# Kernel optimization log

Measured on AMD Instinct MI355X. Metric: run time of the kernel, lower is better.

Reference implementation:

```python
import jax, jax.numpy as jnp
import numpy as np

WS = 8          # window_size
HEADS = 6
DH = 32         # dim_head


def _dwconv(t, w):
    # t: (B,C,H,W), w: (C,1,3,3) depthwise, stride 1, padding 1 -> SAME
    return jax.lax.conv_general_dilated(
        t, w, window_strides=(1, 1), padding='SAME',
        feature_group_count=t.shape[1],
        dimension_numbers=('NCHW', 'OIHW', 'NCHW'))


def _l2norm(t, eps=1e-12):
    # matches F.normalize: x / max(||x||, eps)
    n = jnp.sqrt(jnp.sum(t * t, axis=-1, keepdims=True))
    return t / jnp.maximum(n, eps)


def setup_inputs() -> dict:
    key = jax.random.key(0)
    ks = jax.random.split(key, 10)
    B, H, W, C = 2, 256, 256, 192
    s = 0.05
    return {
        'x': jax.random.normal(ks[0], (B, H, W, C), jnp.float32),
        'illu_fea_trans': jax.random.normal(ks[1], (B, H, W, C), jnp.float32),
        'gt_w': jax.random.normal(ks[2], (C, C), jnp.float32) * s,
        'gt_b': jax.random.normal(ks[3], (C,), jnp.float32) * s,
        'qkv_w': jax.random.normal(ks[4], (C, 3 * C), jnp.float32) * s,
        'qkv_b': jax.random.normal(ks[5], (3 * C,), jnp.float32) * s,
        'proj_w': jax.random.normal(ks[6], (C, C), jnp.float32) * s,
        'proj_b': jax.random.normal(ks[7], (C,), jnp.float32) * s,
        'conv1_w': jax.random.normal(ks[8], (C, 1, 3, 3), jnp.float32) * s,
        'conv2_w': jax.random.normal(ks[9], (C, 1, 3, 3), jnp.float32) * s,
    }


def reference(x, illu_fea_trans, gt_w, gt_b, qkv_w, qkv_b, proj_w, proj_b,
              conv1_w, conv2_w):
    B, H, W, C = x.shape
    Ws, heads, d = WS, HEADS, DH
    scale = d ** (-0.5)
    pad_h = (Ws - H % Ws) % Ws
    pad_w = (Ws - W % Ws) % Ws
    xp = jnp.pad(x, ((0, 0), (0, pad_h), (0, pad_w), (0, 0)), mode='reflect')
    ip = jnp.pad(illu_fea_trans, ((0, 0), (0, pad_h), (0, pad_w), (0, 0)), mode='reflect')
    Hp, Wp = xp.shape[1], xp.shape[2]
    nW = (Hp // Ws) * (Wp // Ws)
    T = Ws * Ws

    def to_windows(t):
        t = t.reshape(B, Hp // Ws, Ws, Wp // Ws, Ws, C)
        return t.transpose(0, 1, 3, 2, 4, 5).reshape(B * nW, T, C)

    xw = to_windows(xp)                                  # (B*nW, T, C)
    qkv = (xw @ qkv_w + qkv_b).reshape(B * nW, T, 3, heads, d)
    qkv = qkv.transpose(2, 0, 3, 1, 4)                   # (3, Bn, h, T, d)
    q, k, v = qkv[0], qkv[1], qkv[2]
    q = _l2norm(q)
    k = _l2norm(k)

    illu = to_windows(ip).reshape(B * nW, T, heads, d).transpose(0, 2, 1, 3)
    v = v * (1.0 + jax.nn.sigmoid(illu))

    # global token: avg-pool over padded spatial dims, then linear
    gt = jnp.mean(xp, axis=(1, 2)) @ gt_w + gt_b          # (B, C)
    gt = gt.reshape(B, heads, 1, d)
    # faithful to torch expand(dim=2 -> nW).reshape(B*nW, heads, 1, d)
    gk = jnp.broadcast_to(gt, (B, heads, nW, d)).reshape(B * nW, heads, 1, d)
    k = jnp.concatenate([k, gk], axis=2)                  # (Bn, h, T+1, d)
    v = jnp.concatenate([v, gk], axis=2)

    # chunked softmax over keys == full softmax over key axis (chunks on q only)
    attn = jax.nn.softmax(jnp.einsum('bhqd,bhkd->bhqk', q, k) * scale, axis=-1)
    out = jnp.einsum('bhqk,bhkd->bhqd', attn, v)          # (Bn, h, T, d)
    out = out.transpose(0, 2, 1, 3).reshape(B * nW, T, C)
    out = out @ proj_w + proj_b

    out = out.reshape(B, Hp // Ws, Wp // Ws, Ws, Ws, C)
    out = out.transpose(0, 1, 3, 2, 4, 5).reshape(B, Hp, Wp, C)[:, :H, :W, :]

    # depthwise-conv positional branch on padded x (exact gelu like torch)
    t = xp.transpose(0, 3, 1, 2)                          # (B,C,Hp,Wp)
    t = _dwconv(t, conv1_w)
    t = jax.nn.gelu(t, approximate=False)
    t = _dwconv(t, conv2_w)
    pos = t.transpose(0, 2, 3, 1)[:, :H, :W, :]
    return out + pos
```

## Files before the change

### kernel.cpp

```cpp
#include <hip/hip_runtime.h>
#include <hip/hip_bf16.h>

#define BB   2
#define HH   256
#define WWD  256
#define CC   192
#define WSZ  8
#define TT   64
#define NHD  6
#define DHD  32
#define N3   576

typedef __attribute__((ext_vector_type(8))) short short8;
typedef __attribute__((ext_vector_type(4))) float f32x4;

__device__ inline short bf16_bits(float f) {
  __hip_bfloat16 h = __float2bfloat16(f);
  return __builtin_bit_cast(short, h);
}

__device__ inline void stage1k(const short* gsrc, short* ldst, int lane) {
  __builtin_amdgcn_global_load_lds(
      (const __attribute__((address_space(1))) void*)(gsrc + lane * 8),
      (__attribute__((address_space(3))) void*)ldst, 16, 0, 0);
}

__global__ __launch_bounds__(256) void lcam_wshuf(const float* __restrict__ src,
                                                  short* __restrict__ dst,
                                                  int ncols, int nfrag, int perm) {
  int gid = blockIdx.x * 256 + threadIdx.x;
  if (gid >= nfrag) return;
  int lane = gid & 63;
  int s = (gid >> 6) % 6;
  int ct = gid / 384;
  int col = ct * 16 + (lane & 15);
  int k0 = s * 32 + (lane >> 4) * 8;
  short8 v;
#pragma unroll
  for (int j = 0; j < 8; ++j)
    v[j] = bf16_bits(src[(size_t)(k0 + j) * ncols + col]);
  int didx = perm ? ((s * (ncols / 16) + ct) * 64 + lane) : gid;
  *(short8*)(dst + (size_t)didx * 8) = v;
}

__global__ __launch_bounds__(256) void lcam_sum_x(const float* __restrict__ x,
                                                  float* __restrict__ sums) {
  int blk = blockIdx.x;
  int b = blk >> 9;
  int chunk = blk & 511;
  const float* xp = x + ((size_t)b * 65536 + (size_t)chunk * 128) * CC;
  int t = threadIdx.x;
  if (t < CC) {
    float acc = 0.f;
    for (int p = 0; p < 128; ++p) acc += xp[(size_t)p * CC + t];
    atomicAdd(&sums[b * CC + t], acc);
  }
}

__global__ void lcam_gt(const float* __restrict__ sums,
                        const float* __restrict__ gt_w,
                        const float* __restrict__ gt_b,
                        float* __restrict__ gt) {
  int b = blockIdx.x;
  int co = threadIdx.x;
  float acc = gt_b[co];
  const float inv = 1.f / 65536.f;
  for (int c = 0; c < CC; ++c)
    acc += sums[b * CC + c] * inv * gt_w[c * CC + co];
  gt[b * CC + co] = acc;
}

__global__ __launch_bounds__(256) void lcam_attn(
    const float* __restrict__ x, const float* __restrict__ illu,
    const short* __restrict__ wf, const short* __restrict__ pwf,
    const float* __restrict__ qkv_b, const float* __restrict__ proj_b,
    const float* __restrict__ gt, float* __restrict__ out) {
  __shared__ __align__(16) short wgt[2][6144];
  __shared__ __align__(16) short ks[65 * 40];
  __shared__ __align__(16) short vt[32 * 72];
  __shared__ __align__(16) short qs[64 * 40];
  __shared__ __align__(16) short ps[64 * 72];

  int w = blockIdx.x;
  int b  = w >> 10;
  int wy = (w >> 5) & 31;
  int wx = w & 31;
  int t  = threadIdx.x;
  int lane = t & 63;
  int rtile = t >> 6;
  int m = lane & 15;
  int quad = lane >> 4;
  int key0 = rtile * 16 + quad * 4;

  size_t base = ((size_t)(b * HH + wy * WSZ) * WWD + wx * WSZ) * CC;

#pragma unroll
  for (int u = 0; u < 3; ++u) {
    int ii = rtile * 3 + u;
    stage1k(wf + ii * 512, wgt[0] + ii * 512, lane);
  }

  int apix = rtile * 16 + m;
  size_t arow = base + (size_t)((apix >> 3) * WWD + (apix & 7)) * CC + quad * 8;
  short8 afrag[6];
#pragma unroll
  for (int s = 0; s < 6; ++s) {
    const float* ap = x + arow + s * 32;
    float4 f0 = *(const float4*)(ap);
    float4 f1 = *(const float4*)(ap + 4);
    short8 v;
    v[0] = bf16_bits(f0.x); v[1] = bf16_bits(f0.y);
    v[2] = bf16_bits(f0.z); v[3] = bf16_bits(f0.w);
    v[4] = bf16_bits(f1.x); v[5] = bf16_bits(f1.y);
    v[6] = bf16_bits(f1.z); v[7] = bf16_bits(f1.w);
    afrag[s] = v;
  }
  const short8* wA8 = (const short8*)wgt[0];
  const short8* wB8 = (const short8*)wgt[1];

  f32x4 pacc[12];
#pragma unroll
  for (int ct = 0; ct < 12; ++ct) {
    f32x4 z = {0.f, 0.f, 0.f, 0.f};
    pacc[ct] = z;
  }

  __syncthreads();

  for (int h = 0; h < NHD; ++h) {
#pragma unroll
    for (int u = 0; u < 3; ++u) {
      int ii = rtile * 3 + u;
      stage1k(wf + (12 + 2 * h) * 3072 + ii * 512, wgt[1] + ii * 512, lane);
    }
    float gv0 = gt[b * CC + h * 32 + m];
    float gv1 = gt[b * CC + h * 32 + 16 + m];
    float il0[4], il1[4];
#pragma unroll
    for (int r = 0; r < 4; ++r) {
      int key = key0 + r;
      const float* ip = illu + base + (size_t)((key >> 3) * WWD + (key & 7)) * CC + h * 32;
      il0[r] = ip[m];
      il1[r] = ip[16 + m];
    }
    {
      f32x4 a0 = {0.f,0.f,0.f,0.f}, a1 = {0.f,0.f,0.f,0.f};
      __builtin_amdgcn_s_setprio(1);
#pragma unroll
      for (int s = 0; s < 6; ++s)
        a0 = __builtin_amdgcn_mfma_f32_16x16x32_bf16(afrag[s], wA8[s*64 + lane], a0, 0,0,0);
#pragma unroll
      for (int s = 0; s < 6; ++s)
        a1 = __builtin_amdgcn_mfma_f32_16x16x32_bf16(afrag[s], wA8[384 + s*64 + lane], a1, 0,0,0);
      __builtin_amdgcn_s_setprio(0);
      float b0 = qkv_b[h*32 + m], b1 = qkv_b[h*32 + 16 + m];
#pragma unroll
      for (int r = 0; r < 4; ++r) {
        float v0 = a0[r] + b0, v1 = a1[r] + b1;
        float ss = v0*v0 + v1*v1;
        ss += __shfl_xor(ss, 1); ss += __shfl_xor(ss, 2);
        ss += __shfl_xor(ss, 4); ss += __shfl_xor(ss, 8);
        float scl = 0.17677669529663688f * __builtin_amdgcn_rsqf(fmaxf(ss, 1e-24f));
        int row = key0 + r;
        qs[row*40 + m]      = bf16_bits(v0 * scl);
        qs[row*40 + 16 + m] = bf16_bits(v1 * scl);
      }
    }
    __syncthreads();
#pragma unroll
    for (int u = 0; u < 3; ++u) {
      int ii = rtile * 3 + u;
      stage1k(wf + (24 + 2 * h) * 3072 + ii * 512, wgt[0] + ii * 512, lane);
    }
    {
      f32x4 a0 = {0.f,0.f,0.f,0.f}, a1 = {0.f,0.f,0.f,0.f};
      __builtin_amdgcn_s_setprio(1);
#pragma unroll
      for (int s = 0; s < 6; ++s)
        a0 = __builtin_amdgcn_mfma_f32_16x16x32_bf16(afrag[s], wB8[s*64 + lane], a0, 0,0,0);
#pragma unroll
      for (int s = 0; s < 6; ++s)
        a1 = __builtin_amdgcn_mfma_f32_16x16x32_bf16(afrag[s], wB8[384 + s*64 + lane], a1, 0,0,0);
      __builtin_amdgcn_s_setprio(0);
      float b0 = qkv_b[192 + h*32 + m], b1 = qkv_b[192 + h*32 + 16 + m];
#pragma unroll
      for (int r = 0; r < 4; ++r) {
        float v0 = a0[r] + b0, v1 = a1[r] + b1;
        float ss = v0*v0 + v1*v1;
        ss += __shfl_xor(ss, 1); ss += __shfl_xor(ss, 2);
        ss += __shfl_xor(ss, 4); ss += __shfl_xor(ss, 8);
        float scl = __builtin_amdgcn_rsqf(fmaxf(ss, 1e-24f));
        int row = key0 + r;
        ks[row*40 + m]      = bf16_bits(v0 * scl);
        ks[row*40 + 16 + m] = bf16_bits(v1 * scl);
      }
    }
    __syncthreads();
#pragma unroll
    for (int u = 0; u < 3; ++u) {
      int ii = rtile * 3 + u;
      stage1k(pwf + h * 6144 + ii * 512, wgt[1] + ii * 512, lane);
    }
    {
      f32x4 a0 = {0.f,0.f,0.f,0.f}, a1 = {0.f,0.f,0.f,0.f};
      __builtin_amdgcn_s_setprio(1);
#pragma unroll
      for (int s = 0; s < 6; ++s)
        a0 = __builtin_amdgcn_mfma_f32_16x16x32_bf16(afrag[s], wA8[s*64 + lane], a0, 0,0,0);
#pragma unroll
      for (int s = 0; s < 6; ++s)
        a1 = __builtin_amdgcn_mfma_f32_16x16x32_bf16(afrag[s], wA8[384 + s*64 + lane], a1, 0,0,0);
      __builtin_amdgcn_s_setprio(0);
      float b0 = qkv_b[384 + h*32 + m], b1 = qkv_b[384 + h*32 + 16 + m];
#pragma unroll
      for (int r = 0; r < 4; ++r) {
        int key = key0 + r;
        float s0 = __builtin_amdgcn_rcpf(1.f + __expf(-il0[r]));
        float s1 = __builtin_amdgcn_rcpf(1.f + __expf(-il1[r]));
        vt[m*72 + key]        = bf16_bits((a0[r] + b0) * (1.f + s0));
        vt[(16 + m)*72 + key] = bf16_bits((a1[r] + b1) * (1.f + s1));
      }
    }
    if (t < DHD) ks[64*40 + t] = bf16_bits(gt[b*CC + h*DHD + t]);
    __syncthreads();
    if (h < NHD - 1) {
#pragma unroll
      for (int u = 0; u < 3; ++u) {
        int ii = rtile * 3 + u;
        stage1k(wf + 2 * (h + 1) * 3072 + ii * 512, wgt[0] + ii * 512, lane);
      }
    }
    short8 qa = *(const short8*)(qs + (rtile*16 + m)*40 + quad*8);
    f32x4 sc[5];
#pragma unroll
    for (int ct = 0; ct < 4; ++ct) {
      short8 kb = *(const short8*)(ks + (ct*16 + m)*40 + quad*8);
      f32x4 z = {0.f,0.f,0.f,0.f};
      sc[ct] = __builtin_amdgcn_mfma_f32_16x16x32_bf16(qa, kb, z, 0,0,0);
    }
    {
      short8 kb = *(const short8*)(ks + 64*40 + quad*8);
      f32x4 z = {0.f,0.f,0.f,0.f};
      sc[4] = __builtin_amdgcn_mfma_f32_16x16x32_bf16(qa, kb, z, 0,0,0);
    }
    float p64v[4], invr[4];
#pragma unroll
    for (int r = 0; r < 4; ++r) {
      float e0 = __expf(sc[0][r]), e1 = __expf(sc[1][r]);
      float e2 = __expf(sc[2][r]), e3 = __expf(sc[3][r]);
      float e4 = (m == 0) ? __expf(sc[4][r]) : 0.f;
      int row = key0 + r;
      ps[row*72 + m]      = bf16_bits(e0);
      ps[row*72 + 16 + m] = bf16_bits(e1);
      ps[row*72 + 32 + m] = bf16_bits(e2);
      ps[row*72 + 48 + m] = bf16_bits(e3);
      float sum = e0 + e1 + e2 + e3 + e4;
      sum += __shfl_xor(sum, 1); sum += __shfl_xor(sum, 2);
      sum += __shfl_xor(sum, 4); sum += __shfl_xor(sum, 8);
      invr[r] = __builtin_amdgcn_rcpf(sum);
      p64v[r] = e4;
    }
    f32x4 o0 = {0.f,0.f,0.f,0.f}, o1 = {0.f,0.f,0.f,0.f};
    __builtin_amdgcn_s_setprio(1);
#pragma unroll
    for (int kc = 0; kc < 2; ++kc) {
      short8 pa  = *(const short8*)(ps + (rtile*16 + m)*72 + kc*32 + quad*8);
      short8 vb0 = *(const short8*)(vt + m*72        + kc*32 + quad*8);
      short8 vb1 = *(const short8*)(vt + (16 + m)*72 + kc*32 + quad*8);
      o0 = __builtin_amdgcn_mfma_f32_16x16x32_bf16(pa, vb0, o0, 0,0,0);
      o1 = __builtin_amdgcn_mfma_f32_16x16x32_bf16(pa, vb1, o1, 0,0,0);
    }
    __builtin_amdgcn_s_setprio(0);
#pragma unroll
    for (int r = 0; r < 4; ++r) {
      float pr = __shfl(p64v[r], lane & 48);
      int row = key0 + r;
      qs[row*40 + m]      = bf16_bits((o0[r] + pr * gv0) * invr[r]);
      qs[row*40 + 16 + m] = bf16_bits((o1[r] + pr * gv1) * invr[r]);
    }
    short8 oa = *(const short8*)(qs + (rtile*16 + m)*40 + quad*8);
    __builtin_amdgcn_s_setprio(1);
#pragma unroll
    for (int ct = 0; ct < 12; ++ct)
      pacc[ct] = __builtin_amdgcn_mfma_f32_16x16x32_bf16(oa, wB8[ct*64 + lane], pacc[ct], 0,0,0);
    __builtin_amdgcn_s_setprio(0);
    __syncthreads();
  }
#pragma unroll
  for (int ct = 0; ct < 12; ++ct) {
    float bias = proj_b[ct*16 + m];
#pragma unroll
    for (int r = 0; r < 4; ++r) {
      int row = key0 + r;
      out[base + (size_t)((row >> 3) * WWD + (row & 7)) * CC + ct*16 + m] = pacc[ct][r] + bias;
    }
  }
}

__global__ __launch_bounds__(256) void lcam_pos(const float* __restrict__ x,
                                                const float* __restrict__ w1,
                                                const float* __restrict__ w2,
                                                float* __restrict__ out) {
  __shared__ __align__(16) float xt[20 * 20 * 16];
  __shared__ float t1[18 * 18 * 16];
  __shared__ float wl1[16 * 9], wl2[16 * 9];
  int blk = blockIdx.x;
  int cgI = blk % 12; int tmp = blk / 12;
  int tx = tmp % 16; tmp /= 16;
  int ty = tmp % 16; int b = tmp / 16;
  int c0 = cgI * 16;
  int y0 = ty * 16, x0 = tx * 16;
  int t = threadIdx.x;
  if (t < 144) { wl1[t] = w1[c0 * 9 + t]; wl2[t] = w2[c0 * 9 + t]; }
  for (int vi = t; vi < 1600; vi += 256) {
    int cc4 = vi & 3;
    int lin = vi >> 2;
    int xx = lin % 20, yy = lin / 20;
    int gy = y0 - 2 + yy, gx = x0 - 2 + xx;
    float4 v = {0.f, 0.f, 0.f, 0.f};
    if (gy >= 0 && gy < HH && gx >= 0 && gx < WWD)
      v = *(const float4*)(x + (((size_t)b * HH + gy) * WWD + gx) * CC + c0 + cc4 * 4);
    *(float4*)(xt + (yy * 20 + xx) * 16 + cc4 * 4) = v;
  }
  __syncthreads();
  for (int idx = t; idx < 5184; idx += 256) {
    int cc = idx & 15;
    int xx = (idx >> 4) % 18;
    int yy = idx / 288;
    int gy = y0 - 1 + yy, gx = x0 - 1 + xx;
    float r = 0.f;
    if (gy >= 0 && gy < HH && gx >= 0 && gx < WWD) {
#pragma unroll
      for (int ky = 0; ky < 3; ++ky)
#pragma unroll
        for (int kx = 0; kx < 3; ++kx)
          r += xt[((yy + ky) * 20 + xx + kx) * 16 + cc] * wl1[cc * 9 + ky * 3 + kx];
      r = 0.5f * r * (1.f + erff(r * 0.70710678118654752f));
    }
    t1[(yy * 18 + xx) * 16 + cc] = r;
  }
  __syncthreads();
  for (int idx = t; idx < 4096; idx += 256) {
    int cc = idx & 15;
    int xx = (idx >> 4) & 15;
    int yy = idx >> 8;
    float r = 0.f;
#pragma unroll
    for (int ky = 0; ky < 3; ++ky)
#pragma unroll
      for (int kx = 0; kx < 3; ++kx)
        r += t1[((yy + ky) * 18 + xx + kx) * 16 + cc] * wl2[cc * 9 + ky * 3 + kx];
    size_t o = (((size_t)b * HH + y0 + yy) * WWD + x0 + xx) * CC + c0 + cc;
    out[o] += r;
  }
}

extern "C" void kernel_launch(void* const* d_in, const int* in_sizes, int n_in,
                              void* d_out, int out_size, void* d_ws, size_t ws_size,
                              hipStream_t stream) {
  const float* x       = (const float*)d_in[0];
  const float* illu    = (const float*)d_in[1];
  const float* gt_w    = (const float*)d_in[2];
  const float* gt_b    = (const float*)d_in[3];
  const float* qkv_w   = (const float*)d_in[4];
  const float* qkv_b   = (const float*)d_in[5];
  const float* proj_w  = (const float*)d_in[6];
  const float* proj_b  = (const float*)d_in[7];
  const float* conv1_w = (const float*)d_in[8];
  const float* conv2_w = (const float*)d_in[9];
  float* out = (float*)d_out;

  short* wf   = (short*)d_ws;
  short* pwf  = (short*)((char*)d_ws + 221184);
  float* sums = (float*)((char*)d_ws + 221184 + 73728);
  float* gt   = sums + BB * CC;

  hipMemsetAsync(sums, 0, BB * CC * sizeof(float), stream);
  lcam_wshuf<<<54, 256, 0, stream>>>(qkv_w, wf, N3, 36 * 6 * 64, 0);
  lcam_wshuf<<<18, 256, 0, stream>>>(proj_w, pwf, CC, 12 * 6 * 64, 1);
  lcam_sum_x<<<1024, 256, 0, stream>>>(x, sums);
  lcam_gt<<<BB, CC, 0, stream>>>(sums, gt_w, gt_b, gt);
  lcam_attn<<<2048, 256, 0, stream>>>(x, illu, wf, pwf, qkv_b, proj_b, gt, out);
  lcam_pos<<<6144, 256, 0, stream>>>(x, conv1_w, conv2_w, out);
}
```

Baseline: 504.4 us.

## Process two attention windows per block to share staged weight tiles

Each 512-thread block now handles two 8x8 windows, with four waves per window. The bf16 QKV and projection weight chunks staged into LDS are shared between both windows, which halves the global-to-LDS weight traffic per window and spreads the staging across eight waves. Per-window scratch buffers (q, k, v, p) are duplicated, which raises LDS use per block. Block-wide barriers now stall both windows together, which may reduce occupancy or scheduling flexibility.

```diff
diff --git a/kernel.cpp b/kernel.cpp
--- a/kernel.cpp
+++ b/kernel.cpp
@@ -70,35 +70,40 @@
   gt[b * CC + co] = acc;
 }
 
-__global__ __launch_bounds__(256) void lcam_attn(
+__global__ __launch_bounds__(512) void lcam_attn(
     const float* __restrict__ x, const float* __restrict__ illu,
     const short* __restrict__ wf, const short* __restrict__ pwf,
     const float* __restrict__ qkv_b, const float* __restrict__ proj_b,
     const float* __restrict__ gt, float* __restrict__ out) {
   __shared__ __align__(16) short wgt[2][6144];
-  __shared__ __align__(16) short ks[65 * 40];
-  __shared__ __align__(16) short vt[32 * 72];
-  __shared__ __align__(16) short qs[64 * 40];
-  __shared__ __align__(16) short ps[64 * 72];
-
-  int w = blockIdx.x;
-  int b  = w >> 10;
-  int wy = (w >> 5) & 31;
-  int wx = w & 31;
-  int t  = threadIdx.x;
+  __shared__ __align__(16) short ks[2][65 * 40];
+  __shared__ __align__(16) short vt[2][32 * 72];
+  __shared__ __align__(16) short qs[2][64 * 40];
+  __shared__ __align__(16) short ps[2][64 * 72];
+
+  int t = threadIdx.x;
   int lane = t & 63;
-  int rtile = t >> 6;
+  int wid = t >> 6;
+  int win = wid >> 2;
+  int rtile = wid & 3;
   int m = lane & 15;
   int quad = lane >> 4;
   int key0 = rtile * 16 + quad * 4;
-
+  int tl = t & 255;
+
+  int wA = blockIdx.x * 2 + win;
+  int b  = wA >> 10;
+  int wy = (wA >> 5) & 31;
+  int wx = wA & 31;
   size_t base = ((size_t)(b * HH + wy * WSZ) * WWD + wx * WSZ) * CC;
 
-#pragma unroll
-  for (int u = 0; u < 3; ++u) {
-    int ii = rtile * 3 + u;
-    stage1k(wf + ii * 512, wgt[0] + ii * 512, lane);
-  }
+  short* ksb = ks[win];
+  short* vtb = vt[win];
+  short* qsb = qs[win];
+  short* psb = ps[win];
+
+  stage1k(wf + wid * 512, wgt[0] + wid * 512, lane);
+  if (wid < 4) stage1k(wf + (wid + 8) * 512, wgt[0] + (wid + 8) * 512, lane);
 
   int apix = rtile * 16 + m;
   size_t arow = base + (size_t)((apix >> 3) * WWD + (apix & 7)) * CC + quad * 8;
@@ -128,10 +133,10 @@
   __syncthreads();
 
   for (int h = 0; h < NHD; ++h) {
-#pragma unroll
-    for (int u = 0; u < 3; ++u) {
-      int ii = rtile * 3 + u;
-      stage1k(wf + (12 + 2 * h) * 3072 + ii * 512, wgt[1] + ii * 512, lane);
+    {
+      const short* g = wf + (12 + 2 * h) * 3072;
+      stage1k(g + wid * 512, wgt[1] + wid * 512, lane);
+      if (wid < 4) stage1k(g + (wid + 8) * 512, wgt[1] + (wid + 8) * 512, lane);
     }
     float gv0 = gt[b * CC + h * 32 + m];
     float gv1 = gt[b * CC + h * 32 + 16 + m];
@@ -162,15 +167,15 @@
         ss += __shfl_xor(ss, 4); ss += __shfl_xor(ss, 8);
         float scl = 0.17677669529663688f * __builtin_amdgcn_rsqf(fmaxf(ss, 1e-24f));
         int row = key0 + r;
-        qs[row*40 + m]      = bf16_bits(v0 * scl);
-        qs[row*40 + 16 + m] = bf16_bits(v1 * scl);
+        qsb[row*40 + m]      = bf16_bits(v0 * scl);
+        qsb[row*40 + 16 + m] = bf16_bits(v1 * scl);
       }
     }
     __syncthreads();
-#pragma unroll
-    for (int u = 0; u < 3; ++u) {
-      int ii = rtile * 3 + u;
-      stage1k(wf + (24 + 2 * h) * 3072 + ii * 512, wgt[0] + ii * 512, lane);
+    {
+      const short* g = wf + (24 + 2 * h) * 3072;
+      stage1k(g + wid * 512, wgt[0] + wid * 512, lane);
+      if (wid < 4) stage1k(g + (wid + 8) * 512, wgt[0] + (wid + 8) * 512, lane);
     }
     {
       f32x4 a0 = {0.f,0.f,0.f,0.f}, a1 = {0.f,0.f,0.f,0.f};
@@ -191,15 +196,15 @@
         ss += __shfl_xor(ss, 4); ss += __shfl_xor(ss, 8);
         float scl = __builtin_amdgcn_rsqf(fmaxf(ss, 1e-24f));
         int row = key0 + r;
-        ks[row*40 + m]      = bf16_bits(v0 * scl);
-        ks[row*40 + 16 + m] = bf16_bits(v1 * scl);
+        ksb[row*40 + m]      = bf16_bits(v0 * scl);
+        ksb[row*40 + 16 + m] = bf16_bits(v1 * scl);
       }
     }
     __syncthreads();
-#pragma unroll
-    for (int u = 0; u < 3; ++u) {
-      int ii = rtile * 3 + u;
-      stage1k(pwf + h * 6144 + ii * 512, wgt[1] + ii * 512, lane);
+    {
+      const short* g = pwf + h * 6144;
+      stage1k(g + wid * 512, wgt[1] + wid * 512, lane);
+      if (wid < 4) stage1k(g + (wid + 8) * 512, wgt[1] + (wid + 8) * 512, lane);
     }
     {
       f32x4 a0 = {0.f,0.f,0.f,0.f}, a1 = {0.f,0.f,0.f,0.f};
@@ -217,29 +222,27 @@
         int key = key0 + r;
         float s0 = __builtin_amdgcn_rcpf(1.f + __expf(-il0[r]));
         float s1 = __builtin_amdgcn_rcpf(1.f + __expf(-il1[r]));
-        vt[m*72 + key]        = bf16_bits((a0[r] + b0) * (1.f + s0));
-        vt[(16 + m)*72 + key] = bf16_bits((a1[r] + b1) * (1.f + s1));
+        vtb[m*72 + key]        = bf16_bits((a0[r] + b0) * (1.f + s0));
+        vtb[(16 + m)*72 + key] = bf16_bits((a1[r] + b1) * (1.f + s1));
       }
     }
-    if (t < DHD) ks[64*40 + t] = bf16_bits(gt[b*CC + h*DHD + t]);
+    if (tl < DHD) ksb[64*40 + tl] = bf16_bits(gt[b*CC + h*DHD + tl]);
     __syncthreads();
     if (h < NHD - 1) {
-#pragma unroll
-      for (int u = 0; u < 3; ++u) {
-        int ii = rtile * 3 + u;
-        stage1k(wf + 2 * (h + 1) * 3072 + ii * 512, wgt[0] + ii * 512, lane);
-      }
-    }
-    short8 qa = *(const short8*)(qs + (rtile*16 + m)*40 + quad*8);
+      const short* g = wf + 2 * (h + 1) * 3072;
+      stage1k(g + wid * 512, wgt[0] + wid * 512, lane);
+      if (wid < 4) stage1k(g + (wid + 8) * 512, wgt[0] + (wid + 8) * 512, lane);
+    }
+    short8 qa = *(const short8*)(qsb + (rtile*16 + m)*40 + quad*8);
     f32x4 sc[5];
 #pragma unroll
     for (int ct = 0; ct < 4; ++ct) {
-      short8 kb = *(const short8*)(ks + (ct*16 + m)*40 + quad*8);
+      short8 kb = *(const short8*)(ksb + (ct*16 + m)*40 + quad*8);
       f32x4 z = {0.f,0.f,0.f,0.f};
       sc[ct] = __builtin_amdgcn_mfma_f32_16x16x32_bf16(qa, kb, z, 0,0,0);
     }
     {
-      short8 kb = *(const short8*)(ks + 64*40 + quad*8);
+      short8 kb = *(const short8*)(ksb + 64*40 + quad*8);
       f32x4 z = {0.f,0.f,0.f,0.f};
       sc[4] = __builtin_amdgcn_mfma_f32_16x16x32_bf16(qa, kb, z, 0,0,0);
     }
@@ -250,10 +253,10 @@
       float e2 = __expf(sc[2][r]), e3 = __expf(sc[3][r]);
       float e4 = (m == 0) ? __expf(sc[4][r]) : 0.f;
       int row = key0 + r;
-      ps[row*72 + m]      = bf16_bits(e0);
-      ps[row*72 + 16 + m] = bf16_bits(e1);
-      ps[row*72 + 32 + m] = bf16_bits(e2);
-      ps[row*72 + 48 + m] = bf16_bits(e3);
+      psb[row*72 + m]      = bf16_bits(e0);
+      psb[row*72 + 16 + m] = bf16_bits(e1);
+      psb[row*72 + 32 + m] = bf16_bits(e2);
+      psb[row*72 + 48 + m] = bf16_bits(e3);
       float sum = e0 + e1 + e2 + e3 + e4;
       sum += __shfl_xor(sum, 1); sum += __shfl_xor(sum, 2);
       sum += __shfl_xor(sum, 4); sum += __shfl_xor(sum, 8);
@@ -264,9 +267,9 @@
     __builtin_amdgcn_s_setprio(1);
 #pragma unroll
     for (int kc = 0; kc < 2; ++kc) {
-      short8 pa  = *(const short8*)(ps + (rtile*16 + m)*72 + kc*32 + quad*8);
-      short8 vb0 = *(const short8*)(vt + m*72        + kc*32 + quad*8);
-      short8 vb1 = *(const short8*)(vt + (16 + m)*72 + kc*32 + quad*8);
+      short8 pa  = *(const short8*)(psb + (rtile*16 + m)*72 + kc*32 + quad*8);
+      short8 vb0 = *(const short8*)(vtb + m*72        + kc*32 + quad*8);
+      short8 vb1 = *(const short8*)(vtb + (16 + m)*72 + kc*32 + quad*8);
       o0 = __builtin_amdgcn_mfma_f32_16x16x32_bf16(pa, vb0, o0, 0,0,0);
       o1 = __builtin_amdgcn_mfma_f32_16x16x32_bf16(pa, vb1, o1, 0,0,0);
     }
@@ -275,10 +278,10 @@
     for (int r = 0; r < 4; ++r) {
       float pr = __shfl(p64v[r], lane & 48);
       int row = key0 + r;
-      qs[row*40 + m]      = bf16_bits((o0[r] + pr * gv0) * invr[r]);
-      qs[row*40 + 16 + m] = bf16_bits((o1[r] + pr * gv1) * invr[r]);
-    }
-    short8 oa = *(const short8*)(qs + (rtile*16 + m)*40 + quad*8);
+      qsb[row*40 + m]      = bf16_bits((o0[r] + pr * gv0) * invr[r]);
+      qsb[row*40 + 16 + m] = bf16_bits((o1[r] + pr * gv1) * invr[r]);
+    }
+    short8 oa = *(const short8*)(qsb + (rtile*16 + m)*40 + quad*8);
     __builtin_amdgcn_s_setprio(1);
 #pragma unroll
     for (int ct = 0; ct < 12; ++ct)
@@ -380,6 +383,6 @@
   lcam_wshuf<<<18, 256, 0, stream>>>(proj_w, pwf, CC, 12 * 6 * 64, 1);
   lcam_sum_x<<<1024, 256, 0, stream>>>(x, sums);
   lcam_gt<<<BB, CC, 0, stream>>>(sums, gt_w, gt_b, gt);
-  lcam_attn<<<2048, 256, 0, stream>>>(x, illu, wf, pwf, qkv_b, proj_b, gt, out);
+  lcam_attn<<<1024, 512, 0, stream>>>(x, illu, wf, pwf, qkv_b, proj_b, gt, out);
   lcam_pos<<<6144, 256, 0, stream>>>(x, conv1_w, conv2_w, out);
 }
```

New measurement: 514.0 us. Within noise of the previous version (+1.9%).
